# Performance work log

Measured on AMD Instinct MI355X. Metric: run time of the kernel, lower is better.

Reference implementation:

```python
import jax, jax.numpy as jnp
import numpy as np

C_ATOM = 128
N_HEADS = 4
HEAD_DIM = C_ATOM // N_HEADS
B, L, A = 16, 2048, 4  # batch, residues, atoms per residue


def setup_inputs() -> dict:
    key = jax.random.key(0)
    ks = jax.random.split(key, 10)
    s = 1.0 / np.sqrt(C_ATOM)
    x = jax.random.normal(ks[0], (B, L, A, C_ATOM), dtype=jnp.float32)
    mask = jax.random.bernoulli(ks[1], 0.9, (B, L, A))
    def lin(kw, kb):
        W = jax.random.uniform(kw, (C_ATOM, C_ATOM), jnp.float32, -s, s)
        b = jax.random.uniform(kb, (C_ATOM,), jnp.float32, -s, s)
        return W, b
    Wq, bq = lin(ks[2], ks[3])
    Wk, bk = lin(ks[4], ks[5])
    Wv, bv = lin(ks[6], ks[7])
    Wo, bo = lin(ks[8], ks[9])
    return {"x": x, "mask": mask, "Wq": Wq, "bq": bq, "Wk": Wk, "bk": bk,
            "Wv": Wv, "bv": bv, "Wo": Wo, "bo": bo}


def reference(x, mask, Wq, bq, Wk, bk, Wv, bv, Wo, bo):
    B_, L_, A_, C = x.shape
    H, D = N_HEADS, HEAD_DIM
    scale = D ** -0.5

    def split_heads(t):  # (B,L,A,C) -> (B,L,H,A,D)
        return t.reshape(B_, L_, A_, H, D).transpose(0, 1, 3, 2, 4)

    q = split_heads(x @ Wq + bq)
    k = split_heads(x @ Wk + bk)
    v = split_heads(x @ Wv + bv)

    # per-residue 4x4 attention scores: (B,L,H,A,A)
    attn = jnp.einsum('blhad,blhed->blhae', q, k) * scale
    # mask keys: mask -> (B,L,1,1,A)
    attn = jnp.where(mask[:, :, None, None, :], attn, -jnp.inf)
    attn = jax.nn.softmax(attn, axis=-1)
    attn = jnp.where(jnp.isnan(attn), 0.0, attn)  # rows with all keys masked

    out = jnp.einsum('blhae,blhed->blhad', attn, v)
    out = out.transpose(0, 1, 3, 2, 4).reshape(B_, L_, A_, C)
    out = out @ Wo + bo
    # zero out residues with no valid atoms
    residue_mask = jnp.any(mask, axis=-1)[..., None, None]  # (B,L,1,1)
    out = out * residue_mask.astype(out.dtype)
    return out
```

## Files before the change

### kernel.cpp

```cpp
#include <hip/hip_runtime.h>
#include <hip/hip_bf16.h>

using f32x4  = __attribute__((ext_vector_type(4))) float;
using bf16x8 = __attribute__((ext_vector_type(8))) short;
typedef unsigned int u32;

__device__ __forceinline__ unsigned short f2bf(float f) {
  u32 u = __float_as_uint(f);
  u += 0x7FFFu + ((u >> 16) & 1u);
  return (unsigned short)(u >> 16);
}

__global__ __launch_bounds__(256) void laa_fused(
    const float* __restrict__ x, const void* __restrict__ maskp,
    const float* __restrict__ Wq, const float* __restrict__ bq,
    const float* __restrict__ Wk, const float* __restrict__ bk,
    const float* __restrict__ Wv, const float* __restrict__ bv,
    const float* __restrict__ Wo, const float* __restrict__ bo,
    float* __restrict__ out, int n_tiles)
{
  constexpr int C = 128;
  __shared__ __align__(128) unsigned short Qlds[16 * 128];
  __shared__ __align__(128) unsigned short Klds[16 * 128];
  __shared__ __align__(128) unsigned short VTlds[128 * 24];
  __shared__ __align__(128) unsigned short Olds[16 * 128];

  const int tid  = threadIdx.x;
  const int wave = tid >> 6;
  const int lane = tid & 63;
  const int c0   = lane & 15;
  const int g    = lane >> 4;

  const u32* mw = (const u32*)maskp;
  u32 det = 0;
  #pragma unroll
  for (int i = 0; i < 64; ++i) det |= mw[i];
  const bool mask_is_byte = (det & 0xFFFFFF00u) != 0u;

  bf16x8 wqf[2][4], wkf[2][4], wvf[2][4], wof[2][4];
  float bq2[2], bk2[2], bv2[2], bo2[2];
  #pragma unroll
  for (int t = 0; t < 2; ++t) {
    const int col = 16 * (2 * wave + t) + c0;
    bq2[t] = bq[col]; bk2[t] = bk[col]; bv2[t] = bv[col]; bo2[t] = bo[col];
    #pragma unroll
    for (int kk = 0; kk < 4; ++kk) {
      const int kb = 32 * kk + 8 * g;
      bf16x8 aq, ak, av, ao;
      #pragma unroll
      for (int j = 0; j < 8; ++j) {
        const int idx = (kb + j) * C + col;
        aq[j] = (short)f2bf(Wq[idx]);
        ak[j] = (short)f2bf(Wk[idx]);
        av[j] = (short)f2bf(Wv[idx]);
        ao[j] = (short)f2bf(Wo[idx]);
      }
      wqf[t][kk] = aq; wkf[t][kk] = ak; wvf[t][kk] = av; wof[t][kk] = ao;
    }
  }

  const float scale = 0.17677669529663687f;

  for (int tile = blockIdx.x; tile < n_tiles; tile += gridDim.x) {
    const int rowbase = tile * 16;
    const float* xt = x + (size_t)rowbase * C;

    bf16x8 af[4];
    #pragma unroll
    for (int kk = 0; kk < 4; ++kk) {
      const float4* p = reinterpret_cast<const float4*>(xt + c0 * C + 32 * kk + 8 * g);
      float4 u0 = p[0], u1 = p[1];
      bf16x8 a;
      a[0]=(short)f2bf(u0.x); a[1]=(short)f2bf(u0.y); a[2]=(short)f2bf(u0.z); a[3]=(short)f2bf(u0.w);
      a[4]=(short)f2bf(u1.x); a[5]=(short)f2bf(u1.y); a[6]=(short)f2bf(u1.z); a[7]=(short)f2bf(u1.w);
      af[kk] = a;
    }

    float kvf[4];
    #pragma unroll
    for (int i = 0; i < 4; ++i) {
      const int idx = rowbase + 4 * g + i;
      const int mv = mask_is_byte ? (int)((const unsigned char*)maskp)[idx]
                                  : ((const int*)maskp)[idx];
      kvf[i] = (mv != 0) ? 1.0f : 0.0f;
    }

    f32x4 qa[2], ka[2], va[2];
    #pragma unroll
    for (int t = 0; t < 2; ++t) {
      qa[t] = f32x4{bq2[t], bq2[t], bq2[t], bq2[t]};
      ka[t] = f32x4{bk2[t], bk2[t], bk2[t], bk2[t]};
      va[t] = f32x4{bv2[t], bv2[t], bv2[t], bv2[t]};
    }
    #pragma unroll
    for (int kk = 0; kk < 4; ++kk) {
      #pragma unroll
      for (int t = 0; t < 2; ++t) {
        qa[t] = __builtin_amdgcn_mfma_f32_16x16x32_bf16(af[kk], wqf[t][kk], qa[t], 0, 0, 0);
        ka[t] = __builtin_amdgcn_mfma_f32_16x16x32_bf16(af[kk], wkf[t][kk], ka[t], 0, 0, 0);
        va[t] = __builtin_amdgcn_mfma_f32_16x16x32_bf16(af[kk], wvf[t][kk], va[t], 0, 0, 0);
      }
    }

    #pragma unroll
    for (int t = 0; t < 2; ++t) {
      const int ch = 16 * (2 * wave + t) + c0;
      #pragma unroll
      for (int i = 0; i < 4; ++i) {
        const int row = 4 * g + i;
        const int off = (row * 256 + ch * 2) ^ ((row & 7) << 4);
        *(unsigned short*)((char*)Qlds + off) = f2bf(qa[t][i] * scale);
        *(unsigned short*)((char*)Klds + off) = f2bf(ka[t][i]);
        VTlds[ch * 24 + row] = f2bf(va[t][i]);
      }
    }

    const int hch = 32 * wave;
    bf16x8 kfrag, qfrag;
    {
      const int row = c0;
      const int chb = hch + 8 * g;
      const int off = (row * 256 + chb * 2) ^ ((row & 7) << 4);
      kfrag = *(const bf16x8*)((const char*)Klds + off);
      qfrag = *(const bf16x8*)((const char*)Qlds + off);
    }
    f32x4 stv = f32x4{0.f, 0.f, 0.f, 0.f};
    stv = __builtin_amdgcn_mfma_f32_16x16x32_bf16(kfrag, qfrag, stv, 0, 0, 0);

    float mx = -1e30f;
    #pragma unroll
    for (int i = 0; i < 4; ++i) if (kvf[i] > 0.f) mx = fmaxf(mx, stv[i]);
    float p[4]; float den = 0.f;
    #pragma unroll
    for (int i = 0; i < 4; ++i) {
      p[i] = (kvf[i] > 0.f && mx > -1e29f) ? __expf(stv[i] - mx) : 0.f;
      den += p[i];
    }
    const float inv = den > 0.f ? 1.0f / den : 0.f;
    const bool diag = ((c0 >> 2) == g);
    u32 p01 = 0u, p23 = 0u;
    if (diag) {
      p01 = (u32)f2bf(p[0] * inv) | ((u32)f2bf(p[1] * inv) << 16);
      p23 = (u32)f2bf(p[2] * inv) | ((u32)f2bf(p[3] * inv) << 16);
    }

    const int srcA = ((2 * g) * 16 + c0) * 4;
    const int srcB = ((2 * g + 1) * 16 + c0) * 4;
    u32 w0 = (u32)__builtin_amdgcn_ds_bpermute(srcA, (int)p01);
    u32 w1 = (u32)__builtin_amdgcn_ds_bpermute(srcA, (int)p23);
    u32 w2 = (u32)__builtin_amdgcn_ds_bpermute(srcB, (int)p01);
    u32 w3 = (u32)__builtin_amdgcn_ds_bpermute(srcB, (int)p23);
    if (g >= 2) { w0 = 0u; w1 = 0u; w2 = 0u; w3 = 0u; }
    bf16x8 pfrag;
    pfrag[0] = (short)(w0 & 0xFFFFu); pfrag[1] = (short)(w0 >> 16);
    pfrag[2] = (short)(w1 & 0xFFFFu); pfrag[3] = (short)(w1 >> 16);
    pfrag[4] = (short)(w2 & 0xFFFFu); pfrag[5] = (short)(w2 >> 16);
    pfrag[6] = (short)(w3 & 0xFFFFu); pfrag[7] = (short)(w3 >> 16);

    f32x4 oa[2];
    oa[0] = f32x4{0.f,0.f,0.f,0.f}; oa[1] = f32x4{0.f,0.f,0.f,0.f};
    #pragma unroll
    for (int nt2 = 0; nt2 < 2; ++nt2) {
      bf16x8 vfrag;
      if (g < 2) {
        const int ch = hch + 16 * nt2 + c0;
        vfrag = *(const bf16x8*)(&VTlds[ch * 24 + 8 * g]);
      } else {
        vfrag[0]=0; vfrag[1]=0; vfrag[2]=0; vfrag[3]=0;
        vfrag[4]=0; vfrag[5]=0; vfrag[6]=0; vfrag[7]=0;
      }
      oa[nt2] = __builtin_amdgcn_mfma_f32_16x16x32_bf16(pfrag, vfrag, oa[nt2], 0, 0, 0);
    }

    #pragma unroll
    for (int nt2 = 0; nt2 < 2; ++nt2) {
      const int ch = hch + 16 * nt2 + c0;
      #pragma unroll
      for (int i = 0; i < 4; ++i) {
        const int row = 4 * g + i;
        const int off = (row * 256 + ch * 2) ^ ((row & 7) << 4);
        *(unsigned short*)((char*)Olds + off) = f2bf(oa[nt2][i]);
      }
    }
    __syncthreads();

    bf16x8 of[4];
    #pragma unroll
    for (int kk = 0; kk < 4; ++kk) {
      const int row = c0;
      const int chb = 32 * kk + 8 * g;
      const int off = (row * 256 + chb * 2) ^ ((row & 7) << 4);
      of[kk] = *(const bf16x8*)((const char*)Olds + off);
    }
    f32x4 fa[2];
    #pragma unroll
    for (int t = 0; t < 2; ++t) fa[t] = f32x4{bo2[t], bo2[t], bo2[t], bo2[t]};
    #pragma unroll
    for (int kk = 0; kk < 4; ++kk) {
      #pragma unroll
      for (int t = 0; t < 2; ++t)
        fa[t] = __builtin_amdgcn_mfma_f32_16x16x32_bf16(of[kk], wof[t][kk], fa[t], 0, 0, 0);
    }

    const float rv = (kvf[0] + kvf[1] + kvf[2] + kvf[3]) > 0.f ? 1.0f : 0.f;
    #pragma unroll
    for (int t = 0; t < 2; ++t) {
      const int ch = 16 * (2 * wave + t) + c0;
      #pragma unroll
      for (int i = 0; i < 4; ++i) {
        const int row = rowbase + 4 * g + i;
        out[(size_t)row * C + ch] = fa[t][i] * rv;
      }
    }
    __syncthreads();
  }
}

extern "C" void kernel_launch(void* const* d_in, const int* in_sizes, int n_in,
                              void* d_out, int out_size, void* d_ws, size_t ws_size,
                              hipStream_t stream) {
  (void)n_in; (void)d_ws; (void)ws_size; (void)out_size;
  const float* x  = (const float*)d_in[0];
  const void* mask = d_in[1];
  const float* Wq = (const float*)d_in[2];
  const float* bq = (const float*)d_in[3];
  const float* Wk = (const float*)d_in[4];
  const float* bk = (const float*)d_in[5];
  const float* Wv = (const float*)d_in[6];
  const float* bv = (const float*)d_in[7];
  const float* Wo = (const float*)d_in[8];
  const float* bo = (const float*)d_in[9];
  float* out = (float*)d_out;

  const int rows = in_sizes[0] / 128;
  const int n_tiles = rows / 16;
  dim3 grid(n_tiles < 512 ? n_tiles : 512), block(256);
  hipLaunchKernelGGL(laa_fused, grid, block, 0, stream,
                     x, mask, Wq, bq, Wk, bk, Wv, bv, Wo, bo, out, n_tiles);
}
```

Measured before the change: 198.8 us.

## Prefetch next tile, double-buffer O LDS, pre-convert weights, enlarge grid

Adds a small pre-kernel that converts the four weight matrices to bf16 in MFMA-fragment order in the workspace, so each block loads its fragments with vector loads instead of strided scalar fp32 loads. Inside the persistent loop, x and mask for the next tile are prefetched into registers while the current tile is computed. The O staging buffer is double-buffered so the trailing barrier can be dropped. The grid grows from 512 to 2048 blocks with launch bounds set for 3 blocks per CU. The cost is a second kernel launch and higher register pressure from the prefetch registers.

```diff
diff --git a/kernel.cpp b/kernel.cpp
--- a/kernel.cpp
+++ b/kernel.cpp
@@ -11,19 +11,36 @@
   return (unsigned short)(u >> 16);
 }
 
-__global__ __launch_bounds__(256) void laa_fused(
+__global__ __launch_bounds__(256) void cvt_weights(
+    const float* __restrict__ Wq, const float* __restrict__ Wk,
+    const float* __restrict__ Wv, const float* __restrict__ Wo,
+    unsigned short* __restrict__ wsT)
+{
+  const int o = blockIdx.x * 256 + threadIdx.x;
+  const int j   = o & 7;
+  const int col = (o >> 3) & 127;
+  const int blk = o >> 10;
+  const int kk  = blk >> 2;
+  const int gg  = blk & 3;
+  const int src = (32 * kk + 8 * gg + j) * 128 + col;
+  wsT[o]             = f2bf(Wq[src]);
+  wsT[16384 + o]     = f2bf(Wk[src]);
+  wsT[32768 + o]     = f2bf(Wv[src]);
+  wsT[49152 + o]     = f2bf(Wo[src]);
+}
+
+__global__ __launch_bounds__(256, 3) void laa_fused(
     const float* __restrict__ x, const void* __restrict__ maskp,
-    const float* __restrict__ Wq, const float* __restrict__ bq,
-    const float* __restrict__ Wk, const float* __restrict__ bk,
-    const float* __restrict__ Wv, const float* __restrict__ bv,
-    const float* __restrict__ Wo, const float* __restrict__ bo,
+    const unsigned short* __restrict__ wsT,
+    const float* __restrict__ bq, const float* __restrict__ bk,
+    const float* __restrict__ bv, const float* __restrict__ bo,
     float* __restrict__ out, int n_tiles)
 {
   constexpr int C = 128;
   __shared__ __align__(128) unsigned short Qlds[16 * 128];
   __shared__ __align__(128) unsigned short Klds[16 * 128];
   __shared__ __align__(128) unsigned short VTlds[128 * 24];
-  __shared__ __align__(128) unsigned short Olds[16 * 128];
+  __shared__ __align__(128) unsigned short Olds[2][16 * 128];
 
   const int tid  = threadIdx.x;
   const int wave = tid >> 6;
@@ -36,6 +53,8 @@
   #pragma unroll
   for (int i = 0; i < 64; ++i) det |= mw[i];
   const bool mask_is_byte = (det & 0xFFFFFF00u) != 0u;
+  const unsigned char* mb = (const unsigned char*)maskp;
+  const int mshift = mask_is_byte ? 0 : 2;
 
   bf16x8 wqf[2][4], wkf[2][4], wvf[2][4], wof[2][4];
   float bq2[2], bk2[2], bv2[2], bo2[2];
@@ -45,45 +64,56 @@
     bq2[t] = bq[col]; bk2[t] = bk[col]; bv2[t] = bv[col]; bo2[t] = bo[col];
     #pragma unroll
     for (int kk = 0; kk < 4; ++kk) {
-      const int kb = 32 * kk + 8 * g;
-      bf16x8 aq, ak, av, ao;
-      #pragma unroll
-      for (int j = 0; j < 8; ++j) {
-        const int idx = (kb + j) * C + col;
-        aq[j] = (short)f2bf(Wq[idx]);
-        ak[j] = (short)f2bf(Wk[idx]);
-        av[j] = (short)f2bf(Wv[idx]);
-        ao[j] = (short)f2bf(Wo[idx]);
-      }
-      wqf[t][kk] = aq; wkf[t][kk] = ak; wvf[t][kk] = av; wof[t][kk] = ao;
+      const int off = (kk * 4 + g) * 1024 + col * 8;
+      wqf[t][kk] = *(const bf16x8*)(wsT + off);
+      wkf[t][kk] = *(const bf16x8*)(wsT + 16384 + off);
+      wvf[t][kk] = *(const bf16x8*)(wsT + 32768 + off);
+      wof[t][kk] = *(const bf16x8*)(wsT + 49152 + off);
     }
   }
 
   const float scale = 0.17677669529663687f;
 
-  for (int tile = blockIdx.x; tile < n_tiles; tile += gridDim.x) {
+  float4 xr[8];
+  int mr[4];
+  auto load_x = [&](int t) {
+    const float* xt = x + (size_t)t * (16 * C) + c0 * C + 8 * g;
+    #pragma unroll
+    for (int kk = 0; kk < 4; ++kk) {
+      const float4* p = reinterpret_cast<const float4*>(xt + 32 * kk);
+      xr[2 * kk]     = p[0];
+      xr[2 * kk + 1] = p[1];
+    }
+  };
+  auto load_m = [&](int t) {
+    const int rb = t * 16 + 4 * g;
+    #pragma unroll
+    for (int i = 0; i < 4; ++i)
+      mr[i] = (int)mb[(size_t)(rb + i) << mshift];
+  };
+
+  int tile = blockIdx.x;
+  if (tile < n_tiles) { load_x(tile); load_m(tile); }
+  int pb = 0;
+
+  for (; tile < n_tiles; tile += gridDim.x) {
     const int rowbase = tile * 16;
-    const float* xt = x + (size_t)rowbase * C;
 
     bf16x8 af[4];
     #pragma unroll
     for (int kk = 0; kk < 4; ++kk) {
-      const float4* p = reinterpret_cast<const float4*>(xt + c0 * C + 32 * kk + 8 * g);
-      float4 u0 = p[0], u1 = p[1];
+      float4 u0 = xr[2 * kk], u1 = xr[2 * kk + 1];
       bf16x8 a;
       a[0]=(short)f2bf(u0.x); a[1]=(short)f2bf(u0.y); a[2]=(short)f2bf(u0.z); a[3]=(short)f2bf(u0.w);
       a[4]=(short)f2bf(u1.x); a[5]=(short)f2bf(u1.y); a[6]=(short)f2bf(u1.z); a[7]=(short)f2bf(u1.w);
       af[kk] = a;
     }
-
     float kvf[4];
     #pragma unroll
-    for (int i = 0; i < 4; ++i) {
-      const int idx = rowbase + 4 * g + i;
-      const int mv = mask_is_byte ? (int)((const unsigned char*)maskp)[idx]
-                                  : ((const int*)maskp)[idx];
-      kvf[i] = (mv != 0) ? 1.0f : 0.0f;
-    }
+    for (int i = 0; i < 4; ++i) kvf[i] = (mr[i] != 0) ? 1.0f : 0.0f;
+
+    const int nxt = tile + (int)gridDim.x;
+    if (nxt < n_tiles) { load_x(nxt); load_m(nxt); }
 
     f32x4 qa[2], ka[2], va[2];
     #pragma unroll
@@ -172,6 +202,7 @@
       oa[nt2] = __builtin_amdgcn_mfma_f32_16x16x32_bf16(pfrag, vfrag, oa[nt2], 0, 0, 0);
     }
 
+    unsigned short* Ob = &Olds[pb][0];
     #pragma unroll
     for (int nt2 = 0; nt2 < 2; ++nt2) {
       const int ch = hch + 16 * nt2 + c0;
@@ -179,7 +210,7 @@
       for (int i = 0; i < 4; ++i) {
         const int row = 4 * g + i;
         const int off = (row * 256 + ch * 2) ^ ((row & 7) << 4);
-        *(unsigned short*)((char*)Olds + off) = f2bf(oa[nt2][i]);
+        *(unsigned short*)((char*)Ob + off) = f2bf(oa[nt2][i]);
       }
     }
     __syncthreads();
@@ -190,7 +221,7 @@
       const int row = c0;
       const int chb = 32 * kk + 8 * g;
       const int off = (row * 256 + chb * 2) ^ ((row & 7) << 4);
-      of[kk] = *(const bf16x8*)((const char*)Olds + off);
+      of[kk] = *(const bf16x8*)((const char*)Ob + off);
     }
     f32x4 fa[2];
     #pragma unroll
@@ -212,14 +243,14 @@
         out[(size_t)row * C + ch] = fa[t][i] * rv;
       }
     }
-    __syncthreads();
+    pb ^= 1;
   }
 }
 
 extern "C" void kernel_launch(void* const* d_in, const int* in_sizes, int n_in,
                               void* d_out, int out_size, void* d_ws, size_t ws_size,
                               hipStream_t stream) {
-  (void)n_in; (void)d_ws; (void)ws_size; (void)out_size;
+  (void)n_in; (void)ws_size; (void)out_size;
   const float* x  = (const float*)d_in[0];
   const void* mask = d_in[1];
   const float* Wq = (const float*)d_in[2];
@@ -231,10 +262,13 @@
   const float* Wo = (const float*)d_in[8];
   const float* bo = (const float*)d_in[9];
   float* out = (float*)d_out;
+  unsigned short* wsT = (unsigned short*)d_ws;
+
+  hipLaunchKernelGGL(cvt_weights, dim3(64), dim3(256), 0, stream, Wq, Wk, Wv, Wo, wsT);
 
   const int rows = in_sizes[0] / 128;
   const int n_tiles = rows / 16;
-  dim3 grid(n_tiles < 512 ? n_tiles : 512), block(256);
-  hipLaunchKernelGGL(laa_fused, grid, block, 0, stream,
-                     x, mask, Wq, bq, Wk, bk, Wv, bv, Wo, bo, out, n_tiles);
-}
+  int grid = n_tiles < 2048 ? n_tiles : 2048;
+  hipLaunchKernelGGL(laa_fused, dim3(grid), dim3(256), 0, stream,
+                     x, mask, wsT, bq, bk, bv, bo, out, n_tiles);
+}
```

After: 329.5 us. 1.66x slower.
